# Kernel tuning notes

Hardware: AMD Instinct MI355X
Metric: run time of the kernel (lower is better)

Reference implementation:

```python
import jax, jax.numpy as jnp
import numpy as np

CHUNK = 64
L2_EPS = 1e-6
RMS_EPS = 1e-5


def _silu(x):
    return x * jax.nn.sigmoid(x)


def _causal_shared_conv(x, w):
    # x: [B,T,C]; w: [K] single kernel shared across all channels (depthwise).
    K = w.shape[0]
    T = x.shape[1]
    xp = jnp.pad(x, ((0, 0), (K - 1, 0), (0, 0)))
    out = w[0] * xp[:, 0:T, :]
    for j in range(1, K):  # K=4, tiny fixed loop
        out = out + w[j] * xp[:, j:j + T, :]
    return out


def _l2norm(x):
    return x * jax.lax.rsqrt(jnp.sum(x * x, axis=-1, keepdims=True) + L2_EPS)


def _delta_rule_chunk(q, k, v, beta, chunk=CHUNK):
    # q,k: [B,H,T,dk]; v: [B,H,T,dv]; beta: [B,H,T]
    B, H, T, dk = q.shape
    dv = v.shape[-1]
    q = q * (dk ** -0.5)
    nC = T // chunk
    q = q.reshape(B, H, nC, chunk, dk)
    k = k.reshape(B, H, nC, chunk, dk)
    v = v.reshape(B, H, nC, chunk, dv)
    beta = beta.reshape(B, H, nC, chunk)
    k_beta = k * beta[..., None]
    v_beta = v * beta[..., None]
    # UT transform: invert the unit-lower-triangular (I + stril(K_beta K^T))
    A = jnp.einsum('bhncd,bhnmd->bhncm', k_beta, k)  # [B,H,nC,C,C]
    stril = jnp.tril(jnp.ones((chunk, chunk), bool), -1)
    M = jnp.where(stril, A, 0.0) + jnp.eye(chunk, dtype=q.dtype)
    u = jax.scipy.linalg.solve_triangular(M, v_beta, lower=True)  # T @ (beta*v)
    w = jax.scipy.linalg.solve_triangular(M, k_beta, lower=True)  # T @ (beta*k)
    tril_incl = jnp.tril(jnp.ones((chunk, chunk), bool))

    def step(S, inp):
        q_i, k_i, u_i, w_i = inp  # [B,H,C,d*]
        u_i = u_i - jnp.einsum('bhcd,bhde->bhce', w_i, S)
        attn = jnp.where(tril_incl, jnp.einsum('bhcd,bhmd->bhcm', q_i, k_i), 0.0)
        o_i = jnp.einsum('bhcd,bhde->bhce', q_i, S) + jnp.einsum('bhcm,bhme->bhce', attn, u_i)
        S = S + jnp.einsum('bhcd,bhce->bhde', k_i, u_i)
        return S, o_i

    xs = tuple(jnp.moveaxis(t, 2, 0) for t in (q, k, u, w))
    S0 = jnp.zeros((B, H, dk, dv), q.dtype)
    _, o = jax.lax.scan(step, S0, xs)  # o: [nC,B,H,C,dv]
    return jnp.moveaxis(o, 0, 2).reshape(B, H, T, dv)


def setup_inputs() -> dict:
    key = jax.random.key(0)
    ks = jax.random.split(key, 10)
    B, T, D, H = 2, 4096, 2048, 16
    sc = 0.02
    return {
        'x': jax.random.normal(ks[0], (B, T, D), jnp.float32),
        'Wq': jax.random.normal(ks[1], (D, D), jnp.float32) * sc,
        'Wk': jax.random.normal(ks[2], (D, D), jnp.float32) * sc,
        'Wv': jax.random.normal(ks[3], (D, D), jnp.float32) * sc,
        'Wb': jax.random.normal(ks[4], (D, H), jnp.float32) * sc,
        'Wo': jax.random.normal(ks[5], (D, D), jnp.float32) * sc,
        'conv_q': jax.random.normal(ks[6], (4,), jnp.float32) * 0.5,
        'conv_k': jax.random.normal(ks[7], (4,), jnp.float32) * 0.5,
        'conv_v': jax.random.normal(ks[8], (4,), jnp.float32) * 0.5,
        'onorm_w': jnp.ones((D // H,), jnp.float32),
    }


def reference(x, Wq, Wk, Wv, Wb, Wo, conv_q, conv_k, conv_v, onorm_w):
    B, T, D = x.shape
    H = Wb.shape[1]
    dk = Wq.shape[1] // H
    dv = Wv.shape[1] // H
    # projections + shared-kernel causal short conv (silu activation)
    q = _silu(_causal_shared_conv(x @ Wq, conv_q))
    k = _silu(_causal_shared_conv(x @ Wk, conv_k))
    v = _silu(_causal_shared_conv(x @ Wv, conv_v))
    beta = jax.nn.sigmoid(x @ Wb)  # [B,T,H]
    # split heads -> [B,H,T,d]
    qh = _l2norm(q.reshape(B, T, H, dk)).transpose(0, 2, 1, 3)
    kh = _l2norm(k.reshape(B, T, H, dk)).transpose(0, 2, 1, 3)
    vh = v.reshape(B, T, H, dv).transpose(0, 2, 1, 3)
    o = _delta_rule_chunk(qh, kh, vh, beta.transpose(0, 2, 1))  # [B,H,T,dv]
    o = o.transpose(0, 2, 1, 3)  # [B,T,H,dv]
    # per-head RMSNorm over head_v_dim
    o = o * jax.lax.rsqrt(jnp.mean(o * o, axis=-1, keepdims=True) + RMS_EPS) * onorm_w
    return o.reshape(B, T, H * dv) @ Wo
```

## Files before the change

kernel.cpp:

```cpp
#include <hip/hip_runtime.h>
#include <math.h>

#define B_ 2
#define T_ 4096
#define D_ 2048
#define H_ 16
#define DK 128
#define DV 128
#define CH 64
#define M_ (B_ * T_)
#define NCH (T_ / CH)

typedef __attribute__((ext_vector_type(8))) short bfrag;
typedef __attribute__((ext_vector_type(4))) float ffrag;
typedef __attribute__((ext_vector_type(8))) unsigned short u16x8;
typedef unsigned short us;

#define MFMA __builtin_amdgcn_mfma_f32_16x16x32_bf16

__device__ inline us f2bf(float f) {
  union { float f; unsigned u; } v; v.f = f;
  unsigned r = v.u + 0x7fffu + ((v.u >> 16) & 1u);
  return (us)(r >> 16);
}
__device__ inline float bf2f(us u) {
  union { unsigned u; float f; } v; v.u = ((unsigned)u) << 16;
  return v.f;
}

__device__ inline void gl_lds16(const us* g, us* l) {
  __builtin_amdgcn_global_load_lds(
      (const __attribute__((address_space(1))) void*)g,
      (__attribute__((address_space(3))) void*)l, 16, 0, 0);
}

__global__ __launch_bounds__(256) void to_bf16(const float* __restrict__ in,
                                               us* __restrict__ out) {
  const size_t i = ((size_t)blockIdx.x * 256 + threadIdx.x) * 8;
  const float4 a = *reinterpret_cast<const float4*>(in + i);
  const float4 b = *reinterpret_cast<const float4*>(in + i + 4);
  ushort4 o0, o1;
  o0.x = f2bf(a.x); o0.y = f2bf(a.y); o0.z = f2bf(a.z); o0.w = f2bf(a.w);
  o1.x = f2bf(b.x); o1.y = f2bf(b.y); o1.z = f2bf(b.z); o1.w = f2bf(b.w);
  *reinterpret_cast<ushort4*>(out + i) = o0;
  *reinterpret_cast<ushort4*>(out + i + 4) = o1;
}

__global__ __launch_bounds__(256) void wtrans(const float* __restrict__ W,
                                              us* __restrict__ Wt) {
  __shared__ float tile[64][68];
  const int k0 = blockIdx.y * 64, n0 = blockIdx.x * 64;
  const int lr = threadIdx.x >> 4, lc = (threadIdx.x & 15) * 4;
#pragma unroll
  for (int p = 0; p < 4; ++p) {
    const int r = lr + p * 16;
    *reinterpret_cast<float4*>(&tile[r][lc]) =
        *reinterpret_cast<const float4*>(&W[(size_t)(k0 + r) * D_ + n0 + lc]);
  }
  __syncthreads();
#pragma unroll
  for (int p = 0; p < 4; ++p) {
    const int r = lr + p * 16;
    ushort4 o;
    o.x = f2bf(tile[lc + 0][r]); o.y = f2bf(tile[lc + 1][r]);
    o.z = f2bf(tile[lc + 2][r]); o.w = f2bf(tile[lc + 3][r]);
    *reinterpret_cast<ushort4*>(&Wt[(size_t)(n0 + r) * D_ + k0 + lc]) = o;
  }
}

template <bool OUTF32>
__global__ __launch_bounds__(256) void gemm_bf16(const us* __restrict__ A,
                                                 const us* __restrict__ Bt,
                                                 void* __restrict__ Cp,
                                                 int M, int N, int K) {
  __shared__ __align__(16) us As[128 * 32];
  __shared__ __align__(16) us Bs[128 * 32];
  const int t = threadIdx.x, l = t & 63, w = t >> 6;
  const int nwg = gridDim.x * gridDim.y;
  const int lin = blockIdx.y * gridDim.x + blockIdx.x;
  const int swz = (lin & 7) * (nwg >> 3) + (lin >> 3);
  const int m0 = (swz / gridDim.x) * 128, n0 = (swz % gridDim.x) * 128;
  const int wr = w >> 1, wc = w & 1;
  const int sr = t >> 2, sp = (t & 3) * 8;
  const int fr = l & 15, fs = (l >> 4) * 8;

  ffrag acc[4][4];
#pragma unroll
  for (int mi = 0; mi < 4; ++mi)
#pragma unroll
    for (int ni = 0; ni < 4; ++ni)
#pragma unroll
      for (int e = 0; e < 4; ++e) acc[mi][ni][e] = 0.f;

  const us* Ag0 = A + (size_t)(m0 + sr) * K + sp;
  const us* Ag1 = A + (size_t)(m0 + sr + 64) * K + sp;
  const us* Bg0 = Bt + (size_t)(n0 + sr) * K + sp;
  const us* Bg1 = Bt + (size_t)(n0 + sr + 64) * K + sp;
  us* Al0 = As + sr * 32 + sp;
  us* Al1 = As + (sr + 64) * 32 + sp;
  us* Bl0 = Bs + sr * 32 + sp;
  us* Bl1 = Bs + (sr + 64) * 32 + sp;

  for (int k0 = 0; k0 < K; k0 += 32) {
    __syncthreads();
    gl_lds16(Ag0 + k0, Al0);
    gl_lds16(Ag1 + k0, Al1);
    gl_lds16(Bg0 + k0, Bl0);
    gl_lds16(Bg1 + k0, Bl1);
    __syncthreads();
    bfrag af[4], bfr[4];
#pragma unroll
    for (int mi = 0; mi < 4; ++mi)
      af[mi] = *reinterpret_cast<const bfrag*>(As + (wr * 64 + mi * 16 + fr) * 32 + fs);
#pragma unroll
    for (int ni = 0; ni < 4; ++ni)
      bfr[ni] = *reinterpret_cast<const bfrag*>(Bs + (wc * 64 + ni * 16 + fr) * 32 + fs);
#pragma unroll
    for (int mi = 0; mi < 4; ++mi)
#pragma unroll
      for (int ni = 0; ni < 4; ++ni)
        acc[mi][ni] = MFMA(af[mi], bfr[ni], acc[mi][ni], 0, 0, 0);
  }
  const int cr = (l >> 4) * 4, cc = l & 15;
#pragma unroll
  for (int mi = 0; mi < 4; ++mi)
#pragma unroll
    for (int ni = 0; ni < 4; ++ni)
#pragma unroll
      for (int j = 0; j < 4; ++j) {
        const size_t idx = (size_t)(m0 + wr * 64 + mi * 16 + cr + j) * N +
                           n0 + wc * 64 + ni * 16 + cc;
        if constexpr (OUTF32) ((float*)Cp)[idx] = acc[mi][ni][j];
        else ((us*)Cp)[idx] = f2bf(acc[mi][ni][j]);
      }
}

__device__ inline void conv_body(const us* __restrict__ in, const float* cw,
                                 int bt, int d0, int mode, float v[8]) {
  const int tb = bt & (T_ - 1);
  const us* row = in + (size_t)bt * D_ + d0;
#pragma unroll
  for (int j = 0; j < 8; ++j) v[j] = 0.f;
#pragma unroll
  for (int j = 0; j < 4; ++j) {
    if (tb >= j) {
      const us* rp = row - (size_t)(j * D_);
      const ushort4 a = *reinterpret_cast<const ushort4*>(rp);
      const ushort4 b = *reinterpret_cast<const ushort4*>(rp + 4);
      const float wj = cw[3 - j];
      v[0] = fmaf(wj, bf2f(a.x), v[0]); v[1] = fmaf(wj, bf2f(a.y), v[1]);
      v[2] = fmaf(wj, bf2f(a.z), v[2]); v[3] = fmaf(wj, bf2f(a.w), v[3]);
      v[4] = fmaf(wj, bf2f(b.x), v[4]); v[5] = fmaf(wj, bf2f(b.y), v[5]);
      v[6] = fmaf(wj, bf2f(b.z), v[6]); v[7] = fmaf(wj, bf2f(b.w), v[7]);
    }
  }
#pragma unroll
  for (int j = 0; j < 8; ++j) v[j] = v[j] / (1.f + expf(-v[j]));
  if (mode) {
    float ss = 0.f;
#pragma unroll
    for (int j = 0; j < 8; ++j) ss = fmaf(v[j], v[j], ss);
    ss += __shfl_xor(ss, 1);
    ss += __shfl_xor(ss, 2);
    ss += __shfl_xor(ss, 4);
    ss += __shfl_xor(ss, 8);
    float sc = rsqrtf(ss + 1e-6f);
    if (mode == 2) sc *= 0.08838834764831845f;
#pragma unroll
    for (int j = 0; j < 8; ++j) v[j] *= sc;
  }
}

__global__ __launch_bounds__(256) void conv_silu_plain(const us* __restrict__ in,
                                                       const float* __restrict__ cw,
                                                       us* __restrict__ out) {
  const int bt = blockIdx.x, d0 = threadIdx.x * 8;
  float v[8];
  conv_body(in, cw, bt, d0, 0, v);
  ushort4 o0, o1;
  o0.x = f2bf(v[0]); o0.y = f2bf(v[1]); o0.z = f2bf(v[2]); o0.w = f2bf(v[3]);
  o1.x = f2bf(v[4]); o1.y = f2bf(v[5]); o1.z = f2bf(v[6]); o1.w = f2bf(v[7]);
  us* op = out + (size_t)bt * D_ + d0;
  *reinterpret_cast<ushort4*>(op) = o0;
  *reinterpret_cast<ushort4*>(op + 4) = o1;
}

__global__ __launch_bounds__(256) void conv_silu_chunk(const us* __restrict__ in,
                                                       const float* __restrict__ cw,
                                                       us* __restrict__ out,
                                                       int mode) {
  const int bt = blockIdx.x, d0 = threadIdx.x * 8;
  float v[8];
  conv_body(in, cw, bt, d0, mode, v);
  const int b = bt >> 12, tt = bt & (T_ - 1);
  const int cid = tt >> 6, r = tt & 63;
  const int h = d0 >> 7, g = (d0 & 127) >> 3;
  us* dst = out + ((size_t)((b * H_ + h) * NCH + cid)) * (CH * DK) +
            r * 128 + ((g ^ (r & 15)) * 8);
  ushort4 o0, o1;
  o0.x = f2bf(v[0]); o0.y = f2bf(v[1]); o0.z = f2bf(v[2]); o0.w = f2bf(v[3]);
  o1.x = f2bf(v[4]); o1.y = f2bf(v[5]); o1.z = f2bf(v[6]); o1.w = f2bf(v[7]);
  *reinterpret_cast<ushort4*>(dst) = o0;
  *reinterpret_cast<ushort4*>(dst + 4) = o1;
}

__global__ __launch_bounds__(256) void beta_sigmoid(const float* __restrict__ x,
                                                    const float* __restrict__ Wb,
                                                    float* __restrict__ betaT) {
  const int t = threadIdx.x;
  const int m = blockIdx.x * 4 + (t >> 6);
  const int l = t & 63;
  const int c = l & 15;
  const int s = l >> 4;
  const float* xr = x + (size_t)m * D_;
  const int kb = s * (D_ / 4);
  float acc = 0.f;
  for (int k = 0; k < D_ / 4; ++k)
    acc = fmaf(xr[kb + k], Wb[(size_t)(kb + k) * H_ + c], acc);
  acc += __shfl_xor(acc, 16);
  acc += __shfl_xor(acc, 32);
  if (l < 16) {
    const int b = m >> 12, tt = m & (T_ - 1);
    betaT[((size_t)(b * H_ + c)) * T_ + tt] = 1.f / (1.f + expf(-acc));
  }
}

__device__ inline void prod_step(float* Tf, const float* Am, float* xbuf,
                                 int r, int c, int I, int J,
                                 int nk, int K0, int K1, int K2) {
  float X = 0.f;
  const int Ks[3] = {K0, K1, K2};
  for (int kk = 0; kk < nk; ++kk) {
    const int K = Ks[kk];
    const float* amrow = Am + (16 * I + r) * 72 + 16 * K;
    const float* tcol = Tf + (16 * K) * 68 + 16 * J + c;
#pragma unroll
    for (int m = 0; m < 16; ++m) X = fmaf(amrow[m], tcol[m * 68], X);
  }
  __syncthreads();
  xbuf[r * 17 + c] = X;
  __syncthreads();
  float s = 0.f;
  const float* trow = Tf + (16 * I + r) * 68 + 16 * I;
#pragma unroll
  for (int m = 0; m < 16; ++m) s = fmaf(trow[m], xbuf[m * 17 + c], s);
  Tf[(16 * I + r) * 68 + 16 * J + c] = -s;
  __syncthreads();
}

__global__ __launch_bounds__(256, 2) void delta_prep(const us* __restrict__ qch,
                                                     const us* __restrict__ kch,
                                                     const float* __restrict__ betaT,
                                                     us* __restrict__ v_uv,
                                                     us* __restrict__ Wout,
                                                     us* __restrict__ kTout,
                                                     us* __restrict__ Aout) {
  __shared__ __align__(16) unsigned char lds[72000];
  us*    ks    = (us*)(lds);
  us*    Tb    = (us*)(lds);
  float* Am    = (float*)(lds + 16384);
  us*    vTb   = (us*)(lds + 16384);
  float* Tf    = (float*)(lds + 34816);
  us*    atst  = (us*)(lds + 34816);
  us*    Wst   = (us*)(lds + 34816);
  us*    kTb   = (us*)(lds + 52224);
  us*    UVst  = (us*)(lds + 52224);
  float* betac = (float*)(lds + 70656);
  float* xbuf  = (float*)(lds + 70912);

  const int t = threadIdx.x, w = t >> 6, l = t & 63;
  const int rr = l & 15, hi = l >> 4;
  const int bx = blockIdx.x;
  const int bh = bx >> 6, cid = bx & 63;
  const int b = bh >> 4, h = bh & 15;
  const size_t rowbase = ((size_t)b * T_ + (size_t)cid * CH) * D_ + (size_t)h * DK;
  const size_t cbase = (size_t)bx * (CH * DK);
  const size_t abase = (size_t)bx * (CH * CH);

  {
    const us* kg = kch + cbase;
#pragma unroll
    for (int p = 0; p < 4; ++p)
      gl_lds16(kg + p * 2048 + t * 8, ks + p * 2048 + t * 8);
    const float4 z = make_float4(0.f, 0.f, 0.f, 0.f);
    *reinterpret_cast<float4*>(atst + t * 16) = z;
    *reinterpret_cast<float4*>(atst + t * 16 + 8) = z;
    if (t < 64) betac[t] = betaT[(size_t)bh * T_ + cid * CH + t];
  }
  __syncthreads();

  {
    bfrag qf[4], kf[4];
#pragma unroll
    for (int k4 = 0; k4 < 4; ++k4) {
      const int go = ((4 * k4 + hi) ^ rr) * 8;
      qf[k4] = *reinterpret_cast<const bfrag*>(qch + cbase + (16 * w + rr) * 128 + go);
      kf[k4] = *reinterpret_cast<const bfrag*>(ks + (16 * w + rr) * 128 + go);
    }
    for (int jt = 0; jt <= w; ++jt) {
      ffrag accA = {0.f, 0.f, 0.f, 0.f}, accQ = {0.f, 0.f, 0.f, 0.f};
#pragma unroll
      for (int k4 = 0; k4 < 4; ++k4) {
        const bfrag bfr = *reinterpret_cast<const bfrag*>(
            ks + (16 * jt + rr) * 128 + (((4 * k4 + hi) ^ rr) * 8));
        accA = MFMA(kf[k4], bfr, accA, 0, 0, 0);
        accQ = MFMA(qf[k4], bfr, accQ, 0, 0, 0);
      }
#pragma unroll
      for (int j4 = 0; j4 < 4; ++j4) {
        const int i = 16 * w + 4 * hi + j4, j = 16 * jt + rr;
        Am[i * 72 + j] = (j < i) ? betac[i] * accA[j4] : 0.f;
        if (j <= i)
          atst[i * 64 + (((j >> 3) ^ (i & 7)) * 8) + (j & 7)] = f2bf(accQ[j4]);
      }
    }
    const int r = t & 63, part = t >> 6;
#pragma unroll
    for (int gi = 0; gi < 4; ++gi) {
      const int g = 4 * part + gi;
      const u16x8 kv = *reinterpret_cast<const u16x8*>(ks + r * 128 + ((g ^ (r & 15)) * 8));
#pragma unroll
      for (int j = 0; j < 8; ++j) kTb[(g * 8 + j) * 72 + r] = kv[j];
    }
  }
  __syncthreads();

  {
#pragma unroll
    for (int p = 0; p < 2; ++p) {
      const int unit = t + p * 256;
      *reinterpret_cast<u16x8*>(Aout + abase + unit * 8) =
          *reinterpret_cast<const u16x8*>(atst + unit * 8);
    }
#pragma unroll
    for (int p = 0; p < 4; ++p) {
      const int unit = t + p * 256;
      const int d = unit >> 3, sg = unit & 7;
      *reinterpret_cast<u16x8*>(kTout + cbase + unit * 8) =
          *reinterpret_cast<const u16x8*>(kTb + d * 72 + ((sg ^ (d & 7)) * 8));
    }
  }
  __syncthreads();
  for (int i = t; i < 64 * 68; i += 256) Tf[i] = 0.f;
  __syncthreads();

  if (t < 64) {
    const int blk = t >> 4, j = t & 15, bd = blk * 16;
    Tf[(bd + j) * 68 + bd + j] = 1.f;
    for (int i = j + 1; i < 16; ++i) {
      float s = 0.f;
      for (int m = j; m < i; ++m)
        s = fmaf(Am[(bd + i) * 72 + bd + m], Tf[(bd + m) * 68 + bd + j], s);
      Tf[(bd + i) * 68 + bd + j] = -s;
    }
  }
  __syncthreads();

  {
    const int r = t >> 4, c = t & 15;
    prod_step(Tf, Am, xbuf, r, c, 1, 0, 1, 0, 0, 0);
    prod_step(Tf, Am, xbuf, r, c, 2, 0, 2, 0, 1, 0);
    prod_step(Tf, Am, xbuf, r, c, 3, 0, 3, 0, 1, 2);
    prod_step(Tf, Am, xbuf, r, c, 2, 1, 1, 1, 0, 0);
    prod_step(Tf, Am, xbuf, r, c, 3, 1, 2, 1, 2, 0);
    prod_step(Tf, Am, xbuf, r, c, 3, 2, 1, 2, 0, 0);
  }

  {
    const int vr = t >> 2, vp = t & 3;
    u16x8 vv[4];
#pragma unroll
    for (int g = 0; g < 4; ++g)
      vv[g] = *reinterpret_cast<const u16x8*>(v_uv + rowbase + (size_t)vr * D_ +
                                              vp * 32 + g * 8);
    const int ti = t >> 2, tg = t & 3;
    u16x8 w0, w1;
#pragma unroll
    for (int jj = 0; jj < 8; ++jj) {
      const int j0 = tg * 16 + jj, j1 = j0 + 8;
      w0[jj] = f2bf(Tf[ti * 68 + j0] * betac[j0]);
      w1[jj] = f2bf(Tf[ti * 68 + j1] * betac[j1]);
    }
    *reinterpret_cast<u16x8*>(Tb + ti * 72 + tg * 16) = w0;
    *reinterpret_cast<u16x8*>(Tb + ti * 72 + tg * 16 + 8) = w1;
#pragma unroll
    for (int g = 0; g < 4; ++g)
#pragma unroll
      for (int j = 0; j < 8; ++j)
        vTb[(vp * 32 + g * 8 + j) * 72 + vr] = vv[g][j];
  }
  __syncthreads();

  {
    bfrag ta[2];
#pragma unroll
    for (int k2 = 0; k2 < 2; ++k2)
      ta[k2] = *reinterpret_cast<const bfrag*>(Tb + (16 * w + rr) * 72 + 32 * k2 + 8 * hi);
#pragma unroll
    for (int dt = 0; dt < 8; ++dt) {
      ffrag acc = {0.f, 0.f, 0.f, 0.f};
#pragma unroll
      for (int k2 = 0; k2 < 2; ++k2) {
        const bfrag bfr = *reinterpret_cast<const bfrag*>(
            kTb + (16 * dt + rr) * 72 + 32 * k2 + 8 * hi);
        acc = MFMA(ta[k2], bfr, acc, 0, 0, 0);
      }
#pragma unroll
      for (int j4 = 0; j4 < 4; ++j4) {
        const int i = 16 * w + 4 * hi + j4, d = 16 * dt + rr;
        Wst[i * 128 + (((d >> 3) ^ (i & 15)) * 8) + (d & 7)] = f2bf(-acc[j4]);
      }
    }
  }
  __syncthreads();

  {
    bfrag ta[2];
#pragma unroll
    for (int k2 = 0; k2 < 2; ++k2)
      ta[k2] = *reinterpret_cast<const bfrag*>(Tb + (16 * w + rr) * 72 + 32 * k2 + 8 * hi);
#pragma unroll
    for (int et = 0; et < 8; ++et) {
      ffrag acc = {0.f, 0.f, 0.f, 0.f};
#pragma unroll
      for (int k2 = 0; k2 < 2; ++k2) {
        const bfrag bfr = *reinterpret_cast<const bfrag*>(
            vTb + (16 * et + rr) * 72 + 32 * k2 + 8 * hi);
        acc = MFMA(ta[k2], bfr, acc, 0, 0, 0);
      }
#pragma unroll
      for (int j4 = 0; j4 < 4; ++j4)
        UVst[(16 * w + 4 * hi + j4) * 128 + 16 * et + rr] = f2bf(acc[j4]);
    }
#pragma unroll
    for (int p = 0; p < 4; ++p) {
      const int unit = t + p * 256;
      *reinterpret_cast<u16x8*>(Wout + cbase + unit * 8) =
          *reinterpret_cast<const u16x8*>(Wst + unit * 8);
    }
  }
  __syncthreads();

#pragma unroll
  for (int p = 0; p < 4; ++p) {
    const int unit = t + p * 256;
    const int r = unit >> 4, g = unit & 15;
    *reinterpret_cast<u16x8*>(v_uv + rowbase + (size_t)r * D_ + g * 8) =
        *reinterpret_cast<const u16x8*>(UVst + r * 128 + g * 8);
  }
}

__global__ __launch_bounds__(256, 1) void delta_seq(const us* __restrict__ qch,
                                                    const us* __restrict__ Wch,
                                                    const us* __restrict__ kTch,
                                                    const us* __restrict__ atch,
                                                    us* __restrict__ uv_o) {
  __shared__ __align__(16) us qs[2][CH * DK];
  __shared__ __align__(16) us Ws[2][CH * DK];
  __shared__ __align__(16) us kTs[2][DK * CH];
  __shared__ __align__(16) us ats[2][CH * CH];
  __shared__ __align__(16) us uvs[2][CH * 16];
  __shared__ __align__(16) us Sb[2][16 * 136];
  __shared__ __align__(16) us ub[CH * 18];

  const int t = threadIdx.x, l = t & 63, w = t >> 6;
  const int bx = blockIdx.x;
  const int vs = bx >> 5, bh = bx & 31;
  const int b = bh >> 4, h = bh & 15;
  const int rr = l & 15, hi = l >> 4;

  ffrag sacc[2];
#pragma unroll
  for (int t2 = 0; t2 < 2; ++t2)
#pragma unroll
    for (int j = 0; j < 4; ++j) sacc[t2][j] = 0.f;

  for (int i = t; i < 16 * 136; i += 256) Sb[0][i] = 0;

  const size_t cbQ = (size_t)(bh * NCH) * (CH * DK);
  const size_t cbA = (size_t)(bh * NCH) * (CH * CH);
  const size_t rowbase0 = ((size_t)b * T_) * D_ + (size_t)h * DK + vs * 16;

#define STAGE(buf, cid)                                                        \
  do {                                                                         \
    const us* qg = qch + cbQ + (size_t)(cid) * (CH * DK);                      \
    const us* Wg = Wch + cbQ + (size_t)(cid) * (CH * DK);                      \
    const us* kg = kTch + cbQ + (size_t)(cid) * (CH * DK);                     \
    const us* ag = atch + cbA + (size_t)(cid) * (CH * CH);                     \
    _Pragma("unroll")                                                          \
    for (int p = 0; p < 4; ++p) {                                              \
      gl_lds16(qg + p * 2048 + t * 8, &qs[buf][p * 2048 + t * 8]);             \
      gl_lds16(Wg + p * 2048 + t * 8, &Ws[buf][p * 2048 + t * 8]);             \
      gl_lds16(kg + p * 2048 + t * 8, &kTs[buf][p * 2048 + t * 8]);            \
    }                                                                          \
    _Pragma("unroll")                                                          \
    for (int p = 0; p < 2; ++p)                                                \
      gl_lds16(ag + p * 2048 + t * 8, &ats[buf][p * 2048 + t * 8]);            \
    if (t < 128)                                                               \
      gl_lds16(uv_o + rowbase0 + (size_t)((cid) * CH + (t >> 1)) * D_ + (t & 1) * 8, \
               &uvs[buf][t * 8]);                                              \
  } while (0)

  STAGE(0, 0);
  asm volatile("s_waitcnt vmcnt(0) lgkmcnt(0)" ::: "memory");
  __builtin_amdgcn_s_barrier();
  __builtin_amdgcn_sched_barrier(0);

  for (int cid = 0; cid < NCH; ++cid) {
    const int cur = cid & 1;
    if (cid + 1 < NCH) STAGE(cur ^ 1, cid + 1);

    bfrag sbf[4];
#pragma unroll
    for (int ks = 0; ks < 4; ++ks)
      sbf[ks] = *reinterpret_cast<const bfrag*>(&Sb[cur][rr * 136 + ks * 32 + hi * 8]);

    {
      ffrag uacc;
#pragma unroll
      for (int j = 0; j < 4; ++j)
        uacc[j] = bf2f(uvs[cur][(16 * w + 4 * hi + j) * 16 + rr]);
#pragma unroll
      for (int ks = 0; ks < 4; ++ks) {
        const bfrag af = *reinterpret_cast<const bfrag*>(
            &Ws[cur][(16 * w + rr) * 128 + (((4 * ks + hi) ^ rr) * 8)]);
        uacc = MFMA(af, sbf[ks], uacc, 0, 0, 0);
      }
#pragma unroll
      for (int j = 0; j < 4; ++j)
        ub[(16 * w + 4 * hi + j) * 18 + rr] = f2bf(uacc[j]);
    }
    asm volatile("s_waitcnt lgkmcnt(0)" ::: "memory");
    __builtin_amdgcn_s_barrier();
    __builtin_amdgcn_sched_barrier(0);

    {
      ffrag oacc;
#pragma unroll
      for (int j = 0; j < 4; ++j) oacc[j] = 0.f;
#pragma unroll
      for (int ks = 0; ks < 4; ++ks) {
        const bfrag af = *reinterpret_cast<const bfrag*>(
            &qs[cur][(16 * w + rr) * 128 + (((4 * ks + hi) ^ rr) * 8)]);
        oacc = MFMA(af, sbf[ks], oacc, 0, 0, 0);
      }
      const int nks = (w < 2) ? 1 : 2;
      for (int ks = 0; ks < nks; ++ks) {
        bfrag ubf;
#pragma unroll
        for (int j = 0; j < 8; ++j)
          ubf[j] = (short)ub[(32 * ks + 8 * hi + j) * 18 + rr];
        const bfrag af = *reinterpret_cast<const bfrag*>(
            &ats[cur][(16 * w + rr) * 64 + (((4 * ks + hi) ^ (rr & 7)) * 8)]);
        oacc = MFMA(af, ubf, oacc, 0, 0, 0);
      }
      us* og = uv_o + rowbase0 + (size_t)(cid * CH) * D_;
#pragma unroll
      for (int j = 0; j < 4; ++j)
        og[(size_t)(16 * w + 4 * hi + j) * D_ + rr] = f2bf(oacc[j]);
    }

    {
      bfrag ubf[2];
#pragma unroll
      for (int ks = 0; ks < 2; ++ks)
#pragma unroll
        for (int j = 0; j < 8; ++j)
          ubf[ks][j] = (short)ub[(32 * ks + 8 * hi + j) * 18 + rr];
#pragma unroll
      for (int t2 = 0; t2 < 2; ++t2) {
        const int tile = 2 * w + t2;
#pragma unroll
        for (int ks = 0; ks < 2; ++ks) {
          const bfrag af = *reinterpret_cast<const bfrag*>(
              &kTs[cur][(16 * tile + rr) * 64 + (((4 * ks + hi) ^ (rr & 7)) * 8)]);
          sacc[t2] = MFMA(af, ubf[ks], sacc[t2], 0, 0, 0);
        }
        ushort4 sw;
        sw.x = f2bf(sacc[t2][0]); sw.y = f2bf(sacc[t2][1]);
        sw.z = f2bf(sacc[t2][2]); sw.w = f2bf(sacc[t2][3]);
        *reinterpret_cast<ushort4*>(&Sb[cur ^ 1][rr * 136 + 16 * tile + 4 * hi]) = sw;
      }
    }
    asm volatile("s_waitcnt vmcnt(0) lgkmcnt(0)" ::: "memory");
    __builtin_amdgcn_s_barrier();
    __builtin_amdgcn_sched_barrier(0);
  }
#undef STAGE
}

__global__ __launch_bounds__(256) void rms_onorm_bf16(const us* __restrict__ in,
                                                      const float* __restrict__ w,
                                                      us* __restrict__ out) {
  const int bt = blockIdx.x;
  const int d0 = threadIdx.x * 8;
  const us* p = in + (size_t)bt * D_ + d0;
  const ushort4 a = *reinterpret_cast<const ushort4*>(p);
  const ushort4 b = *reinterpret_cast<const ushort4*>(p + 4);
  float v[8] = {bf2f(a.x), bf2f(a.y), bf2f(a.z), bf2f(a.w),
                bf2f(b.x), bf2f(b.y), bf2f(b.z), bf2f(b.w)};
  float ss = 0.f;
#pragma unroll
  for (int j = 0; j < 8; ++j) ss = fmaf(v[j], v[j], ss);
  ss += __shfl_xor(ss, 1);
  ss += __shfl_xor(ss, 2);
  ss += __shfl_xor(ss, 4);
  ss += __shfl_xor(ss, 8);
  const float sc = rsqrtf(ss * (1.0f / 128.0f) + 1e-5f);
  const int hd = d0 & 127;
  ushort4 o0, o1;
  o0.x = f2bf(v[0] * sc * w[hd + 0]); o0.y = f2bf(v[1] * sc * w[hd + 1]);
  o0.z = f2bf(v[2] * sc * w[hd + 2]); o0.w = f2bf(v[3] * sc * w[hd + 3]);
  o1.x = f2bf(v[4] * sc * w[hd + 4]); o1.y = f2bf(v[5] * sc * w[hd + 5]);
  o1.z = f2bf(v[6] * sc * w[hd + 6]); o1.w = f2bf(v[7] * sc * w[hd + 7]);
  us* op = out + (size_t)bt * D_ + d0;
  *reinterpret_cast<ushort4*>(op) = o0;
  *reinterpret_cast<ushort4*>(op + 4) = o1;
}

extern "C" void kernel_launch(void* const* d_in, const int* in_sizes, int n_in,
                              void* d_out, int out_size, void* d_ws, size_t ws_size,
                              hipStream_t stream) {
  const float* x  = (const float*)d_in[0];
  const float* Wq = (const float*)d_in[1];
  const float* Wk = (const float*)d_in[2];
  const float* Wv = (const float*)d_in[3];
  const float* Wb = (const float*)d_in[4];
  const float* Wo = (const float*)d_in[5];
  const float* cq = (const float*)d_in[6];
  const float* ck = (const float*)d_in[7];
  const float* cv = (const float*)d_in[8];
  const float* ow = (const float*)d_in[9];
  float* out = (float*)d_out;

  const size_t NE = (size_t)M_ * D_;
  us* ws   = (us*)d_ws;
  us* gout = ws;
  us* qch  = ws + NE;
  us* kch  = ws + 2 * NE;
  us* Wch  = ws + 3 * NE;
  us* kTch = ws + 4 * NE;
  us* wt   = ws + 5 * NE;
  us* attb = gout;
  float* betaT = (float*)(gout + 12 * 1024 * 1024);
  us* xb = (us*)d_out;
  us* vb = xb + NE;

  dim3 gg(D_ / 128, M_ / 128);
  dim3 wg(D_ / 64, D_ / 64);

  to_bf16<<<NE / 2048, 256, 0, stream>>>(x, xb);

  wtrans<<<wg, 256, 0, stream>>>(Wv, wt);
  gemm_bf16<false><<<gg, 256, 0, stream>>>(xb, wt, gout, M_, D_, D_);
  conv_silu_plain<<<M_, 256, 0, stream>>>(gout, cv, vb);

  wtrans<<<wg, 256, 0, stream>>>(Wq, wt);
  gemm_bf16<false><<<gg, 256, 0, stream>>>(xb, wt, gout, M_, D_, D_);
  conv_silu_chunk<<<M_, 256, 0, stream>>>(gout, cq, qch, 2);

  wtrans<<<wg, 256, 0, stream>>>(Wk, wt);
  gemm_bf16<false><<<gg, 256, 0, stream>>>(xb, wt, gout, M_, D_, D_);
  conv_silu_chunk<<<M_, 256, 0, stream>>>(gout, ck, kch, 1);

  beta_sigmoid<<<M_ / 4, 256, 0, stream>>>(x, Wb, betaT);

  delta_prep<<<32 * NCH, 256, 0, stream>>>(qch, kch, betaT, vb, Wch, kTch, attb);
  delta_seq<<<256, 256, 0, stream>>>(qch, Wch, kTch, attb, vb);

  rms_onorm_bf16<<<M_, 256, 0, stream>>>(vb, ow, kTch);

  wtrans<<<wg, 256, 0, stream>>>(Wo, wt);
  gemm_bf16<true><<<gg, 256, 0, stream>>>(kTch, wt, out, M_, D_, D_);
}
```

Baseline: 786.5 us.

## Replace GEMM with 256x256 tile, triple-buffered LDS pipeline and swizzled layout

Replaces the 128x128 single-buffered bf16 GEMM with a 256x256-tile, 512-thread kernel. It uses a three-stage LDS ring with direct global-to-LDS prefetch two steps ahead, XOR-swizzled LDS columns to avoid bank conflicts, and split MFMA phases with priority hints. The aim is to hide global load latency and raise MFMA utilisation in the four large projection GEMMs. In exchange the grid is much smaller (256 workgroups) and per-thread register use is higher.

```diff
diff --git a/kernel.cpp b/kernel.cpp
--- a/kernel.cpp
+++ b/kernel.cpp
@@ -69,67 +69,126 @@
 }
 
 template <bool OUTF32>
-__global__ __launch_bounds__(256) void gemm_bf16(const us* __restrict__ A,
-                                                 const us* __restrict__ Bt,
-                                                 void* __restrict__ Cp,
-                                                 int M, int N, int K) {
-  __shared__ __align__(16) us As[128 * 32];
-  __shared__ __align__(16) us Bs[128 * 32];
+__global__ __launch_bounds__(512, 2) void gemm256(const us* __restrict__ A,
+                                                  const us* __restrict__ Bt,
+                                                  void* __restrict__ Cp,
+                                                  int M, int N, int K) {
+  __shared__ __align__(16) us lA[3][256 * 32];
+  __shared__ __align__(16) us lB[3][256 * 32];
   const int t = threadIdx.x, l = t & 63, w = t >> 6;
-  const int nwg = gridDim.x * gridDim.y;
-  const int lin = blockIdx.y * gridDim.x + blockIdx.x;
+  const int wm = w >> 2, wn = w & 3;
+  const int fr = l & 15, hi = l >> 4;
+  const int colx = 8 * (hi ^ ((fr >> 2) & 3));
+
+  const int nx = gridDim.x;
+  const int nwg = nx * gridDim.y;
+  const int lin = blockIdx.y * nx + blockIdx.x;
   const int swz = (lin & 7) * (nwg >> 3) + (lin >> 3);
-  const int m0 = (swz / gridDim.x) * 128, n0 = (swz % gridDim.x) * 128;
-  const int wr = w >> 1, wc = w & 1;
-  const int sr = t >> 2, sp = (t & 3) * 8;
-  const int fr = l & 15, fs = (l >> 4) * 8;
-
-  ffrag acc[4][4];
-#pragma unroll
-  for (int mi = 0; mi < 4; ++mi)
+  const int m0 = (swz / nx) * 256, n0 = (swz % nx) * 256;
+
+  const int srow = t >> 2;
+  const int csrc = ((t & 3) * 8) ^ (((t >> 4) & 3) * 8);
+  const us* Asrc0 = A + (size_t)(m0 + srow) * K + csrc;
+  const us* Asrc1 = A + (size_t)(m0 + 128 + srow) * K + csrc;
+  const us* Bsrc0 = Bt + (size_t)(n0 + srow) * K + csrc;
+  const us* Bsrc1 = Bt + (size_t)(n0 + 128 + srow) * K + csrc;
+
+  ffrag acc[8][4];
+#pragma unroll
+  for (int mi = 0; mi < 8; ++mi)
 #pragma unroll
     for (int ni = 0; ni < 4; ++ni)
 #pragma unroll
       for (int e = 0; e < 4; ++e) acc[mi][ni][e] = 0.f;
 
-  const us* Ag0 = A + (size_t)(m0 + sr) * K + sp;
-  const us* Ag1 = A + (size_t)(m0 + sr + 64) * K + sp;
-  const us* Bg0 = Bt + (size_t)(n0 + sr) * K + sp;
-  const us* Bg1 = Bt + (size_t)(n0 + sr + 64) * K + sp;
-  us* Al0 = As + sr * 32 + sp;
-  us* Al1 = As + (sr + 64) * 32 + sp;
-  us* Bl0 = Bs + sr * 32 + sp;
-  us* Bl1 = Bs + (sr + 64) * 32 + sp;
-
-  for (int k0 = 0; k0 < K; k0 += 32) {
-    __syncthreads();
-    gl_lds16(Ag0 + k0, Al0);
-    gl_lds16(Ag1 + k0, Al1);
-    gl_lds16(Bg0 + k0, Bl0);
-    gl_lds16(Bg1 + k0, Bl1);
-    __syncthreads();
-    bfrag af[4], bfr[4];
+#define SA_(bufp, g)                                              \
+  do {                                                            \
+    gl_lds16(Asrc0 + (size_t)(g) * 32, (bufp) + t * 8);           \
+    gl_lds16(Asrc1 + (size_t)(g) * 32, (bufp) + 4096 + t * 8);    \
+  } while (0)
+#define SB_(bufp, g)                                              \
+  do {                                                            \
+    gl_lds16(Bsrc0 + (size_t)(g) * 32, (bufp) + t * 8);           \
+    gl_lds16(Bsrc1 + (size_t)(g) * 32, (bufp) + 4096 + t * 8);    \
+  } while (0)
+
+  const int NT = K >> 5;
+  us* const baseA = &lA[0][0];
+  us* const baseB = &lB[0][0];
+
+  SA_(baseA, 0); SB_(baseB, 0);
+  SA_(baseA + 8192, 1); SB_(baseB + 8192, 1);
+  asm volatile("s_waitcnt vmcnt(4)" ::: "memory");
+  __builtin_amdgcn_s_barrier();
+  __builtin_amdgcn_sched_barrier(0);
+
+  int cur = 0, nxt = 2;
+  const int rbA = wm * 128 + fr;
+  const int rbB = wn * 64 + fr;
+
+#pragma unroll 1
+  for (int g = 0; g < NT; ++g) {
+    us* const curA = baseA + cur * 8192;
+    us* const curB = baseB + cur * 8192;
+    us* const nxtA = baseA + nxt * 8192;
+    us* const nxtB = baseB + nxt * 8192;
+
+    bfrag bf4[4], af4[4];
+#pragma unroll
+    for (int ni = 0; ni < 4; ++ni)
+      bf4[ni] = *reinterpret_cast<const bfrag*>(curB + (rbB + ni * 16) * 32 + colx);
 #pragma unroll
     for (int mi = 0; mi < 4; ++mi)
-      af[mi] = *reinterpret_cast<const bfrag*>(As + (wr * 64 + mi * 16 + fr) * 32 + fs);
+      af4[mi] = *reinterpret_cast<const bfrag*>(curA + (rbA + mi * 16) * 32 + colx);
+    if (g + 2 < NT) SA_(nxtA, g + 2);
+    __builtin_amdgcn_s_barrier();
+    asm volatile("s_waitcnt lgkmcnt(0)" ::: "memory");
+    __builtin_amdgcn_sched_barrier(0);
+    __builtin_amdgcn_s_setprio(1);
+#pragma unroll
+    for (int mi = 0; mi < 4; ++mi)
+#pragma unroll
+      for (int ni = 0; ni < 4; ++ni)
+        acc[mi][ni] = MFMA(af4[mi], bf4[ni], acc[mi][ni], 0, 0, 0);
+    __builtin_amdgcn_s_setprio(0);
+    __builtin_amdgcn_s_barrier();
+
+#pragma unroll
+    for (int mi = 0; mi < 4; ++mi)
+      af4[mi] = *reinterpret_cast<const bfrag*>(curA + (rbA + (mi + 4) * 16) * 32 + colx);
+    if (g + 2 < NT) SB_(nxtB, g + 2);
+    __builtin_amdgcn_s_barrier();
+    asm volatile("s_waitcnt lgkmcnt(0)" ::: "memory");
+    __builtin_amdgcn_sched_barrier(0);
+    __builtin_amdgcn_s_setprio(1);
+#pragma unroll
+    for (int mi = 0; mi < 4; ++mi)
+#pragma unroll
+      for (int ni = 0; ni < 4; ++ni)
+        acc[mi + 4][ni] = MFMA(af4[mi], bf4[ni], acc[mi + 4][ni], 0, 0, 0);
+    __builtin_amdgcn_s_setprio(0);
+    if (g + 2 < NT)
+      asm volatile("s_waitcnt vmcnt(4)" ::: "memory");
+    else
+      asm volatile("s_waitcnt vmcnt(0)" ::: "memory");
+    __builtin_amdgcn_s_barrier();
+    __builtin_amdgcn_sched_barrier(0);
+
+    cur = (cur == 2) ? 0 : cur + 1;
+    nxt = (nxt == 2) ? 0 : nxt + 1;
+  }
+#undef SA_
+#undef SB_
+
+  const int crow = m0 + wm * 128 + 4 * hi;
+  const int ccol = n0 + wn * 64 + fr;
+#pragma unroll
+  for (int mi = 0; mi < 8; ++mi)
 #pragma unroll
     for (int ni = 0; ni < 4; ++ni)
-      bfr[ni] = *reinterpret_cast<const bfrag*>(Bs + (wc * 64 + ni * 16 + fr) * 32 + fs);
-#pragma unroll
-    for (int mi = 0; mi < 4; ++mi)
-#pragma unroll
-      for (int ni = 0; ni < 4; ++ni)
-        acc[mi][ni] = MFMA(af[mi], bfr[ni], acc[mi][ni], 0, 0, 0);
-  }
-  const int cr = (l >> 4) * 4, cc = l & 15;
-#pragma unroll
-  for (int mi = 0; mi < 4; ++mi)
-#pragma unroll
-    for (int ni = 0; ni < 4; ++ni)
 #pragma unroll
       for (int j = 0; j < 4; ++j) {
-        const size_t idx = (size_t)(m0 + wr * 64 + mi * 16 + cr + j) * N +
-                           n0 + wc * 64 + ni * 16 + cc;
+        const size_t idx = (size_t)(crow + mi * 16 + j) * N + ccol + ni * 16;
         if constexpr (OUTF32) ((float*)Cp)[idx] = acc[mi][ni][j];
         else ((us*)Cp)[idx] = f2bf(acc[mi][ni][j]);
       }
@@ -646,21 +705,21 @@
   us* xb = (us*)d_out;
   us* vb = xb + NE;
 
-  dim3 gg(D_ / 128, M_ / 128);
+  dim3 gg(D_ / 256, M_ / 256);
   dim3 wg(D_ / 64, D_ / 64);
 
   to_bf16<<<NE / 2048, 256, 0, stream>>>(x, xb);
 
   wtrans<<<wg, 256, 0, stream>>>(Wv, wt);
-  gemm_bf16<false><<<gg, 256, 0, stream>>>(xb, wt, gout, M_, D_, D_);
+  gemm256<false><<<gg, 512, 0, stream>>>(xb, wt, gout, M_, D_, D_);
   conv_silu_plain<<<M_, 256, 0, stream>>>(gout, cv, vb);
 
   wtrans<<<wg, 256, 0, stream>>>(Wq, wt);
-  gemm_bf16<false><<<gg, 256, 0, stream>>>(xb, wt, gout, M_, D_, D_);
+  gemm256<false><<<gg, 512, 0, stream>>>(xb, wt, gout, M_, D_, D_);
   conv_silu_chunk<<<M_, 256, 0, stream>>>(gout, cq, qch, 2);
 
   wtrans<<<wg, 256, 0, stream>>>(Wk, wt);
-  gemm_bf16<false><<<gg, 256, 0, stream>>>(xb, wt, gout, M_, D_, D_);
+  gemm256<false><<<gg, 512, 0, stream>>>(xb, wt, gout, M_, D_, D_);
   conv_silu_chunk<<<M_, 256, 0, stream>>>(gout, ck, kch, 1);
 
   beta_sigmoid<<<M_ / 4, 256, 0, stream>>>(x, Wb, betaT);
@@ -671,5 +730,5 @@
   rms_onorm_bf16<<<M_, 256, 0, stream>>>(vb, ow, kTch);
 
   wtrans<<<wg, 256, 0, stream>>>(Wo, wt);
-  gemm_bf16<true><<<gg, 256, 0, stream>>>(kTch, wt, out, M_, D_, D_);
-}
+  gemm256<true><<<gg, 512, 0, stream>>>(kTch, wt, out, M_, D_, D_);
+}
```

Result: faster. 677.7 us (-13.8%).
